# Kernel tuning notes

Hardware: AMD Instinct MI355X
Metric: run time of the kernel (lower is better)

Reference implementation:

```python
import jax, jax.numpy as jnp
import numpy as np

H = 4       # num_heads (forced == num_gates by reshape math in source)
G = 4       # num_gates
HID = 1024  # hidden_size
D = HID // H  # head_dim = 256
T = 512     # sequence length
B = 16      # batch


def setup_inputs() -> dict:
    key = jax.random.key(0)
    k1, k2, k3 = jax.random.split(key, 3)
    lim = 1.0 / np.sqrt(HID)
    # x holds pre-projected gate preactivations Wx: [T, B, 4*hidden]
    x = jax.random.normal(k1, (T, B, G * HID), dtype=jnp.float32) * 0.1
    recurrent_kernel = jax.random.uniform(k2, (H, D, G, D), dtype=jnp.float32, minval=-lim, maxval=lim)
    bias = jax.random.uniform(k3, (H, G, D), dtype=jnp.float32, minval=-lim, maxval=lim)
    return {"x": x, "recurrent_kernel": recurrent_kernel, "bias": bias}


def reference(x, recurrent_kernel, bias):
    # Reproduce the source's reshape chain (valid since H == G == 4):
    # rk: [H, D, G, D] -> permute(0,2,3,1) -> [H, G, D, D] -> reshape(H, D, H*D)
    rk1 = jnp.transpose(recurrent_kernel, (0, 2, 3, 1)).reshape(H, D, H * D)
    # transpose(1,2) -> [H, H*D, D] -> reshape(H, D, G*D)
    rk2 = jnp.swapaxes(rk1, 1, 2).reshape(H, D, G * D)
    bflat = bias.reshape(-1)  # head-major flatten, as in source
    Bsz = x.shape[1]
    zero = jnp.zeros((Bsz, HID), dtype=x.dtype)

    def step(carry, Wx_t):
        h, c, n, m = carry
        # Ry: [B,H,1,D] @ [1,H,D,G*D] -> [B,H,G*D] -> [B,H,G,D] -> [B,G,H,D] -> [B, G*HID]
        Ry = jnp.einsum('bhd,hdg->bhg', h.reshape(Bsz, H, D), rk2)
        Ry = Ry.reshape(Bsz, H, G, D).transpose(0, 2, 1, 3).reshape(Bsz, -1)
        raw = (Wx_t + Ry + bflat).reshape(Bsz, G, HID)
        iraw, fraw, zraw, oraw = raw[:, 0], raw[:, 1], raw[:, 2], raw[:, 3]
        logfplusm = m + jax.nn.log_sigmoid(fraw)
        # source: if all(n == 0): mnew = iraw else max(iraw, logfplusm)
        mnew = jnp.where(jnp.all(n == 0.0), iraw, jnp.maximum(iraw, logfplusm))
        ogate = jax.nn.sigmoid(oraw)
        igate = jnp.exp(iraw - mnew)
        fgate = jnp.exp(logfplusm - mnew)
        cnew = fgate * c + igate * jnp.tanh(zraw)
        nnew = fgate * h + igate  # faithful to source (uses hidden_state, not n)
        hnew = ogate * cnew / nnew
        return (hnew, cnew, nnew, mnew), hnew

    carry0 = (zero, zero, zero, zero)
    (hT, cT, nT, mT), outs = jax.lax.scan(step, carry0, x)
    # output = all_states[0][1:] (hidden over time), state = all_states[:, -1]
    final_state = jnp.stack((hT, cT, nT, mT), axis=0)
    return outs, final_state
```

## Files before the change

kernel.cpp:

```cpp
#include <hip/hip_runtime.h>
#include <hip/hip_fp16.h>
#include <stdint.h>


#define NTS 512
#define OUTS_ELEMS (NTS * 16 * 1024)
#define SPIN_CAP 8192

typedef _Float16 half2v __attribute__((ext_vector_type(2)));

__device__ __forceinline__ float fdot2f(uint32_t a, uint32_t b, float c) {
#if __has_builtin(__builtin_amdgcn_fdot2)
  union U { uint32_t u; half2v h; };
  U ua, ub; ua.u = a; ub.u = b;
  return __builtin_amdgcn_fdot2(ua.h, ub.h, c, false);
#else
  __half2 ha, hb;
  *(uint32_t*)&ha = a; *(uint32_t*)&hb = b;
  float2 fa = __half22float2(ha), fb = __half22float2(hb);
  return fmaf(fa.y, fb.y, fmaf(fa.x, fb.x, c));
#endif
}

__device__ __forceinline__ float qxor1(float v) {
  return __int_as_float(__builtin_amdgcn_update_dpp(
      0, __float_as_int(v), 0xB1, 0xF, 0xF, true));
}
__device__ __forceinline__ float qxor2(float v) {
  return __int_as_float(__builtin_amdgcn_update_dpp(
      0, __float_as_int(v), 0x4E, 0xF, 0xF, true));
}

__global__ void repack_weights(const float* __restrict__ rk,
                               uint32_t* __restrict__ wp) {
  int tid = blockIdx.x * 256 + threadIdx.x;
  int dd   = tid & 3;
  int lane = (tid >> 2) & 63;
  int mm   = (tid >> 8) & 31;
  int W    = tid >> 13;
  int head = W >> 4, ww = W & 15;
  int jl = lane >> 2, kq = lane & 3;
  int n = mm * 4 + dd;
  int g = n >> 5, p = n & 31;
  int dout = ww * 16 + jl;
  uint32_t word = 0;
  #pragma unroll
  for (int e = 0; e < 2; ++e) {
    int klo = 2 * p + e;
    float v = rk[head * 262144 + (klo * 4 + g) * 1024 +
                 (dout >> 6) * 256 + (dout & 63) * 4 + kq];
    word |= (uint32_t)__half_as_ushort(__float2half(v)) << (16 * e);
  }
  wp[tid] = word;
}

__global__ __launch_bounds__(256, 1) void slstm_main(
    const float* __restrict__ x, const float* __restrict__ bias,
    const uint32_t* __restrict__ wp, uint32_t* hex,
    float* __restrict__ out) {
  __shared__ __align__(16) uint32_t lhp[4][144];

  const int bid = blockIdx.x;
  const int xcd = bid & 7, yy = bid >> 3;
  const int q4 = yy & 3, ii = yy >> 2;
  const int cc = xcd * 8 + ii;
  const int b = cc >> 2, head = cc & 3;
  const int lane = threadIdx.x & 63, w = threadIdx.x >> 6;
  const int ww = q4 * 4 + w;
  const int jl = lane >> 2, kq = lane & 3;
  const int dout = ww * 16 + jl;

  const uint4* wp4 = (const uint4*)wp;
  const int base = (head * 16 + ww) * 2048 + lane;
#define LDW(i) uint4 wv##i = wp4[base + (i) * 64]
  LDW(0);  LDW(1);  LDW(2);  LDW(3);  LDW(4);  LDW(5);  LDW(6);  LDW(7);
  LDW(8);  LDW(9);  LDW(10); LDW(11); LDW(12); LDW(13); LDW(14); LDW(15);
  LDW(16); LDW(17); LDW(18); LDW(19); LDW(20); LDW(21); LDW(22); LDW(23);
  LDW(24); LDW(25); LDW(26); LDW(27); LDW(28); LDW(29); LDW(30); LDW(31);
#undef LDW
#define LAU(i) asm volatile("" : "+v"(wv##i.x), "+v"(wv##i.y), \
                                 "+v"(wv##i.z), "+v"(wv##i.w))
  LAU(0);  LAU(1);  LAU(2);  LAU(3);  LAU(4);  LAU(5);  LAU(6);  LAU(7);
  LAU(8);  LAU(9);  LAU(10); LAU(11); LAU(12); LAU(13); LAU(14); LAU(15);
  LAU(16); LAU(17); LAU(18); LAU(19); LAU(20); LAU(21); LAU(22); LAU(23);
  LAU(24); LAU(25); LAU(26); LAU(27); LAU(28); LAU(29); LAU(30); LAU(31);
#undef LAU

  const float bg = bias[kq * 1024 + head * 256 + dout];
  const int xoff0 = b * 4096 + kq * 1024 + head * 256 + dout;
  float xv = x[xoff0];

  const int rd_base = cc * 256 + lane * 4;
  const int wr_idx  = cc * 256 + dout;
  const int out_off = b * 1024 + head * 256 + dout;
  const bool pub = (kq == 0);

  uint32_t* lrow = &lhp[w][0];
  const int widx = (lane >> 4) * 36 + ((2 * lane) & 31);

  float hs = 0.f, cs = 0.f, nns = 0.f, ms = 0.f;

  #pragma unroll 1
  for (int t = 0; t < NTS; ++t) {
    float xb = xv + bg;
    float A0 = (kq == 0) ? xb : 0.f;
    float A1 = (kq == 1) ? xb : 0.f;
    float A2 = (kq == 2) ? xb : 0.f;
    float A3 = (kq == 3) ? xb : 0.f;
    float xn = 0.f;
    if (t > 0) {
      const uint32_t tg = (uint32_t)t;
      const uint32_t* sp = hex + ((t - 1) & 1) * 16384 + rd_base;
      uint32_t v0, v1, v2, v3; int spins = 0;
      for (;;) {
        v0 = __hip_atomic_load(sp + 0, __ATOMIC_RELAXED, __HIP_MEMORY_SCOPE_AGENT);
        v1 = __hip_atomic_load(sp + 1, __ATOMIC_RELAXED, __HIP_MEMORY_SCOPE_AGENT);
        v2 = __hip_atomic_load(sp + 2, __ATOMIC_RELAXED, __HIP_MEMORY_SCOPE_AGENT);
        v3 = __hip_atomic_load(sp + 3, __ATOMIC_RELAXED, __HIP_MEMORY_SCOPE_AGENT);
        int ok = ((v0 & 0xffffu) == tg) & ((v1 & 0xffffu) == tg) &
                 ((v2 & 0xffffu) == tg) & ((v3 & 0xffffu) == tg);
        if (__all(ok)) break;
        if (++spins > SPIN_CAP) break;
      }
      if (t < NTS - 1) xn = x[xoff0 + (t + 1) * 65536];
      uint32_t p0 = (v0 >> 16) | (v1 & 0xffff0000u);
      uint32_t p1 = (v2 >> 16) | (v3 & 0xffff0000u);
      *(uint64_t*)&lrow[widx] = ((uint64_t)p1 << 32) | (uint64_t)p0;
      const uint4* rp = (const uint4*)&lrow[kq * 36];
#define DOTSTEP(c, W0, W1, W2, W3)                  \
      do {                                          \
        uint4 hw = rp[c];                           \
        A0 = fdot2f(W0.x, hw.x, A0);                \
        A0 = fdot2f(W0.y, hw.y, A0);                \
        A0 = fdot2f(W0.z, hw.z, A0);                \
        A0 = fdot2f(W0.w, hw.w, A0);                \
        A1 = fdot2f(W1.x, hw.x, A1);                \
        A1 = fdot2f(W1.y, hw.y, A1);                \
        A1 = fdot2f(W1.z, hw.z, A1);                \
        A1 = fdot2f(W1.w, hw.w, A1);                \
        A2 = fdot2f(W2.x, hw.x, A2);                \
        A2 = fdot2f(W2.y, hw.y, A2);                \
        A2 = fdot2f(W2.z, hw.z, A2);                \
        A2 = fdot2f(W2.w, hw.w, A2);                \
        A3 = fdot2f(W3.x, hw.x, A3);                \
        A3 = fdot2f(W3.y, hw.y, A3);                \
        A3 = fdot2f(W3.z, hw.z, A3);                \
        A3 = fdot2f(W3.w, hw.w, A3);                \
      } while (0)
      DOTSTEP(0, wv0, wv8,  wv16, wv24);
      DOTSTEP(1, wv1, wv9,  wv17, wv25);
      DOTSTEP(2, wv2, wv10, wv18, wv26);
      DOTSTEP(3, wv3, wv11, wv19, wv27);
      DOTSTEP(4, wv4, wv12, wv20, wv28);
      DOTSTEP(5, wv5, wv13, wv21, wv29);
      DOTSTEP(6, wv6, wv14, wv22, wv30);
      DOTSTEP(7, wv7, wv15, wv23, wv31);
#undef DOTSTEP
    } else {
      xn = x[xoff0 + 65536];
    }

    A0 += qxor1(A0); A0 += qxor2(A0);
    A1 += qxor1(A1); A1 += qxor2(A1);
    A2 += qxor1(A2); A2 += qxor2(A2);
    A3 += qxor1(A3); A3 += qxor2(A3);

    float ri = A0, rf = A1, rz = A2, ro = A3;
    float lsf = fminf(rf, 0.f) - __logf(1.f + __expf(-fabsf(rf)));
    float lf = ms + lsf;
    float mnew = (t == 0) ? ri : fmaxf(ri, lf);
    float ig = __expf(ri - mnew);
    float fg = __expf(lf - mnew);
    float e2z = __expf(2.f * rz);
    float tz = 1.f - 2.f / (e2z + 1.f);
    float cnew = fg * cs + ig * tz;
    float nnew = fg * hs + ig;
    float hnew = cnew / ((1.f + __expf(-ro)) * nnew);
    hs = hnew; cs = cnew; nns = nnew; ms = mnew;

    unsigned short hf = __half_as_ushort(__float2half(hnew));
    if (pub) {
      uint32_t wword = ((uint32_t)hf << 16) | (uint32_t)(t + 1);
      __hip_atomic_store(hex + (t & 1) * 16384 + wr_idx, wword,
                         __ATOMIC_RELAXED, __HIP_MEMORY_SCOPE_AGENT);
      out[t * 16384 + out_off] = hnew;
    }
    xv = xn;
  }

  if (pub) {
    float* fs = out + OUTS_ELEMS;
    fs[out_off] = hs;
    fs[16384 + out_off] = cs;
    fs[32768 + out_off] = nns;
    fs[49152 + out_off] = ms;
  }
}

extern "C" void kernel_launch(void* const* d_in, const int* in_sizes, int n_in,
                              void* d_out, int out_size, void* d_ws,
                              size_t ws_size, hipStream_t stream) {
  const float* x    = (const float*)d_in[0];
  const float* rk   = (const float*)d_in[1];
  const float* bias = (const float*)d_in[2];
  uint32_t* wp  = (uint32_t*)d_ws;
  uint32_t* hex = (uint32_t*)((char*)d_ws + (1u << 21));
  float* out = (float*)d_out;

  repack_weights<<<2048, 256, 0, stream>>>(rk, wp);
  slstm_main<<<256, 256, 0, stream>>>(x, bias, wp, hex, out);
}
```

Before: 836.6 us.

## Add fast-path dwordx4 sc0 polling buffer for cross-block hidden-state exchange

Adds a second exchange buffer that each producer writes with a raw sc0 store and that consumers poll with a single 16-byte sc0 load per iteration, instead of four separate agent-scope atomic loads. If the fast path fails to observe the data within a bounded number of polls, that block permanently falls back to the original atomic buffer, which is still written every step. The aim is to cut the per-step inter-block synchronization latency that dominates the sequential recurrence. It relies on sc0 cache semantics for cross-CU visibility on this hardware, and it adds an extra store per step.

```diff
diff --git a/kernel.cpp b/kernel.cpp
--- a/kernel.cpp
+++ b/kernel.cpp
@@ -5,6 +5,7 @@
 
 #define NTS 512
 #define OUTS_ELEMS (NTS * 16 * 1024)
+#define FAST_CAP 256
 #define SPIN_CAP 8192
 
 typedef _Float16 half2v __attribute__((ext_vector_type(2)));
@@ -29,6 +30,14 @@
 __device__ __forceinline__ float qxor2(float v) {
   return __int_as_float(__builtin_amdgcn_update_dpp(
       0, __float_as_int(v), 0x4E, 0xF, 0xF, true));
+}
+
+__device__ __forceinline__ uint4 poll16(const uint32_t* p) {
+  uint4 r;
+  asm volatile("global_load_dwordx4 %0, %1, off sc0\n\t"
+               "s_waitcnt vmcnt(0)"
+               : "=v"(r) : "v"(p) : "memory");
+  return r;
 }
 
 __global__ void repack_weights(const float* __restrict__ rk,
@@ -56,7 +65,7 @@
 
 __global__ __launch_bounds__(256, 1) void slstm_main(
     const float* __restrict__ x, const float* __restrict__ bias,
-    const uint32_t* __restrict__ wp, uint32_t* hex,
+    const uint32_t* __restrict__ wp, uint32_t* hexS, uint32_t* hexF,
     float* __restrict__ out) {
   __shared__ __align__(16) uint32_t lhp[4][144];
 
@@ -99,6 +108,7 @@
   const int widx = (lane >> 4) * 36 + ((2 * lane) & 31);
 
   float hs = 0.f, cs = 0.f, nns = 0.f, ms = 0.f;
+  int useFast = 1;
 
   #pragma unroll 1
   for (int t = 0; t < NTS; ++t) {
@@ -110,17 +120,33 @@
     float xn = 0.f;
     if (t > 0) {
       const uint32_t tg = (uint32_t)t;
-      const uint32_t* sp = hex + ((t - 1) & 1) * 16384 + rd_base;
-      uint32_t v0, v1, v2, v3; int spins = 0;
-      for (;;) {
-        v0 = __hip_atomic_load(sp + 0, __ATOMIC_RELAXED, __HIP_MEMORY_SCOPE_AGENT);
-        v1 = __hip_atomic_load(sp + 1, __ATOMIC_RELAXED, __HIP_MEMORY_SCOPE_AGENT);
-        v2 = __hip_atomic_load(sp + 2, __ATOMIC_RELAXED, __HIP_MEMORY_SCOPE_AGENT);
-        v3 = __hip_atomic_load(sp + 3, __ATOMIC_RELAXED, __HIP_MEMORY_SCOPE_AGENT);
-        int ok = ((v0 & 0xffffu) == tg) & ((v1 & 0xffffu) == tg) &
-                 ((v2 & 0xffffu) == tg) & ((v3 & 0xffffu) == tg);
-        if (__all(ok)) break;
-        if (++spins > SPIN_CAP) break;
+      const int slot = ((t - 1) & 1) * 16384 + rd_base;
+      uint32_t v0 = 0, v1 = 0, v2 = 0, v3 = 0;
+      int got = 0;
+      if (useFast) {
+        const uint32_t* spF = hexF + slot;
+        for (int it = 0; it < FAST_CAP; ++it) {
+          uint4 v = poll16(spF);
+          int ok = ((v.x & 0xffffu) == tg) & ((v.y & 0xffffu) == tg) &
+                   ((v.z & 0xffffu) == tg) & ((v.w & 0xffffu) == tg);
+          if (__all(ok)) { v0 = v.x; v1 = v.y; v2 = v.z; v3 = v.w;
+                           got = 1; break; }
+        }
+        if (!got) useFast = 0;
+      }
+      if (!got) {
+        const uint32_t* sp = hexS + slot;
+        int spins = 0;
+        for (;;) {
+          v0 = __hip_atomic_load(sp + 0, __ATOMIC_RELAXED, __HIP_MEMORY_SCOPE_AGENT);
+          v1 = __hip_atomic_load(sp + 1, __ATOMIC_RELAXED, __HIP_MEMORY_SCOPE_AGENT);
+          v2 = __hip_atomic_load(sp + 2, __ATOMIC_RELAXED, __HIP_MEMORY_SCOPE_AGENT);
+          v3 = __hip_atomic_load(sp + 3, __ATOMIC_RELAXED, __HIP_MEMORY_SCOPE_AGENT);
+          int ok = ((v0 & 0xffffu) == tg) & ((v1 & 0xffffu) == tg) &
+                   ((v2 & 0xffffu) == tg) & ((v3 & 0xffffu) == tg);
+          if (__all(ok)) break;
+          if (++spins > SPIN_CAP) break;
+        }
       }
       if (t < NTS - 1) xn = x[xoff0 + (t + 1) * 65536];
       uint32_t p0 = (v0 >> 16) | (v1 & 0xffff0000u);
@@ -181,7 +207,10 @@
     unsigned short hf = __half_as_ushort(__float2half(hnew));
     if (pub) {
       uint32_t wword = ((uint32_t)hf << 16) | (uint32_t)(t + 1);
-      __hip_atomic_store(hex + (t & 1) * 16384 + wr_idx, wword,
+      uint32_t* pF = hexF + (t & 1) * 16384 + wr_idx;
+      asm volatile("global_store_dword %0, %1, off sc0"
+                   :: "v"(pF), "v"(wword) : "memory");
+      __hip_atomic_store(hexS + (t & 1) * 16384 + wr_idx, wword,
                          __ATOMIC_RELAXED, __HIP_MEMORY_SCOPE_AGENT);
       out[t * 16384 + out_off] = hnew;
     }
@@ -203,10 +232,11 @@
   const float* x    = (const float*)d_in[0];
   const float* rk   = (const float*)d_in[1];
   const float* bias = (const float*)d_in[2];
-  uint32_t* wp  = (uint32_t*)d_ws;
-  uint32_t* hex = (uint32_t*)((char*)d_ws + (1u << 21));
+  uint32_t* wp   = (uint32_t*)d_ws;
+  uint32_t* hexS = (uint32_t*)((char*)d_ws + (1u << 21));
+  uint32_t* hexF = (uint32_t*)((char*)d_ws + (1u << 21) + (1u << 17));
   float* out = (float*)d_out;
 
   repack_weights<<<2048, 256, 0, stream>>>(rk, wp);
-  slstm_main<<<256, 256, 0, stream>>>(x, bias, wp, hex, out);
-}
+  slstm_main<<<256, 256, 0, stream>>>(x, bias, wp, hexS, hexF, out);
+}
```

New measurement: 875.2 us. 1.05x slower.
